# Kernel tuning notes

Hardware: AMD Instinct MI355X
Metric: run time of the kernel (lower is better)

The kernel has to match this reference:

```python
import jax, jax.numpy as jnp
import numpy as np

B, N, C, H, NRES = 32, 1024, 384, 1024, 20
NTAB = 21  # 20 aa + unknown, per AlphaFold residue_constants


def setup_inputs() -> dict:
    key = jax.random.key(0)
    ks = jax.random.split(key, 16)
    s = 0.02
    inp = {}
    inp['act'] = jax.random.normal(ks[0], (B, N, C), jnp.float32)
    inp['angles'] = jax.random.normal(ks[1], (B, N, 7, 2), jnp.float32)
    inp['rigids'] = jax.random.normal(ks[2], (B, N, 7), jnp.float32)
    inp['fixed_mask'] = jax.random.randint(ks[3], (B, N), 0, 2, jnp.int32)
    inp['seq_t'] = jax.random.randint(ks[4], (B, N), 0, NRES, jnp.int32)
    inp['residx_atom37_to_atom14'] = jax.random.randint(ks[5], (B, N, 37), 0, 14, jnp.int32)
    inp['ln_g'] = jnp.ones((C,), jnp.float32)
    inp['ln_b'] = jnp.zeros((C,), jnp.float32)
    inp['w1'] = jax.random.normal(ks[6], (C, H), jnp.float32) * s
    inp['b1'] = jnp.zeros((H,), jnp.float32)
    inp['w2'] = jax.random.normal(ks[7], (H, H), jnp.float32) * s
    inp['b2'] = jnp.zeros((H,), jnp.float32)
    inp['w3'] = jax.random.normal(ks[8], (H, NRES), jnp.float32) * s
    inp['b3'] = jnp.zeros((NRES,), jnp.float32)
    # stand-in residue_constants tables (same shapes/dtypes as AlphaFold's)
    inp['default_frames'] = jax.random.normal(ks[9], (NTAB, 8, 4, 4), jnp.float32)
    inp['group_idx'] = jax.random.randint(ks[10], (NTAB, 14), 0, 8, jnp.int32)
    inp['atom14_mask'] = (jax.random.uniform(ks[11], (NTAB, 14)) > 0.3).astype(jnp.float32)
    inp['atom37_mask'] = (jax.random.uniform(ks[12], (NTAB, 37)) > 0.3).astype(jnp.float32)
    inp['lit_positions'] = jax.random.normal(ks[13], (NTAB, 14, 3), jnp.float32)
    return inp


def quat_to_rot(q):
    q = q / jnp.sqrt(jnp.sum(q * q, axis=-1, keepdims=True) + 1e-8)
    w, x, y, z = q[..., 0], q[..., 1], q[..., 2], q[..., 3]
    r = jnp.stack([
        1 - 2 * (y * y + z * z), 2 * (x * y - w * z), 2 * (x * z + w * y),
        2 * (x * y + w * z), 1 - 2 * (x * x + z * z), 2 * (y * z - w * x),
        2 * (x * z - w * y), 2 * (y * z + w * x), 1 - 2 * (x * x + y * y)
    ], axis=-1)
    return r.reshape(q.shape[:-1] + (3, 3))


def compose(r1, t1, r2, t2):
    # rigid composition: (r1, t1) o (r2, t2)
    return (jnp.einsum('...ij,...jk->...ik', r1, r2),
            jnp.einsum('...ij,...j->...i', r1, t2) + t1)


def reference(act, angles, rigids, fixed_mask, seq_t, residx_atom37_to_atom14,
              ln_g, ln_b, w1, b1, w2, b2, w3, b3,
              default_frames, group_idx, atom14_mask, atom37_mask, lit_positions):
    # --- small MLP head ---
    mu = jnp.mean(act, axis=-1, keepdims=True)
    var = jnp.var(act, axis=-1, keepdims=True)
    h = (act - mu) / jnp.sqrt(var + 1e-5) * ln_g + ln_b
    h = jax.nn.relu(h @ w1 + b1)
    h = jax.nn.relu(h @ w2 + b2)
    logits = h @ w3 + b3                                # [B,N,20]
    p_0t = jax.nn.softmax(logits, axis=-1)
    seq0 = jnp.argmax(p_0t, axis=-1).astype(jnp.int32)
    seq0 = seq0 * (1 - fixed_mask) + seq_t * fixed_mask  # [B,N]

    # --- backbone frame from quaternion rigids ---
    rb = quat_to_rot(rigids[..., :4])                    # [B,N,3,3]
    tb = rigids[..., 4:]                                 # [B,N,3]

    # --- torsion_angles_to_frames ---
    df = default_frames[seq0]                            # [B,N,8,4,4]
    dr, dt = df[..., :3, :3], df[..., :3, 3]
    sin, cos = angles[..., 0], angles[..., 1]            # [B,N,7]
    z1 = jnp.zeros_like(sin[..., :1])
    sin8 = jnp.concatenate([z1, sin], axis=-1)           # backbone group has angle 0
    cos8 = jnp.concatenate([jnp.ones_like(z1), cos], axis=-1)
    zz, oo = jnp.zeros_like(sin8), jnp.ones_like(sin8)
    rx = jnp.stack([oo, zz, zz, zz, cos8, -sin8, zz, sin8, cos8], axis=-1)
    rx = rx.reshape(sin8.shape + (3, 3))                 # rotation about x-axis
    fr = jnp.einsum('bngij,bngjk->bngik', dr, rx)        # frames to backbone (pre-chain)
    ft = dt
    # chain chi2->chi1, chi3->chi2, chi4->chi3
    r5, t5 = compose(fr[..., 4, :, :], ft[..., 4, :], fr[..., 5, :, :], ft[..., 5, :])
    r6, t6 = compose(r5, t5, fr[..., 6, :, :], ft[..., 6, :])
    r7, t7 = compose(r6, t6, fr[..., 7, :, :], ft[..., 7, :])
    frot = jnp.concatenate([fr[..., :5, :, :], r5[..., None, :, :], r6[..., None, :, :], r7[..., None, :, :]], axis=-3)
    ftr = jnp.concatenate([ft[..., :5, :], t5[..., None, :], t6[..., None, :], t7[..., None, :]], axis=-2)
    grot, gtr = compose(rb[..., None, :, :], tb[..., None, :], frot, ftr)  # [B,N,8,3,3],[B,N,8,3]

    # --- frames_and_literature_positions_to_atom14_pos ---
    gi = group_idx[seq0]                                 # [B,N,14]
    ar = jnp.take_along_axis(grot, jnp.broadcast_to(gi[..., None, None], gi.shape + (3, 3)), axis=2)
    at = jnp.take_along_axis(gtr, jnp.broadcast_to(gi[..., None], gi.shape + (3,)), axis=2)
    lit = lit_positions[seq0]                            # [B,N,14,3]
    m14 = atom14_mask[seq0]                              # [B,N,14]
    pred = (jnp.einsum('bnaij,bnaj->bnai', ar, lit) + at) * m14[..., None]

    # --- atom14 -> atom37 gather ---
    idx = residx_atom37_to_atom14
    final = jnp.take_along_axis(pred, jnp.broadcast_to(idx[..., None], idx.shape + (3,)), axis=2)
    m37 = atom37_mask[seq0]                              # [B,N,37]
    return logits, seq0, pred, final, m14, m37
```

## Files before the change

### kernel.cpp

```cpp
#include <hip/hip_runtime.h>
#include <math.h>

#define B_ 32
#define N_ 1024
#define C_ 384
#define H_ 1024
#define NRES 20
#define NTAB 21
#define M_TOTAL (B_*N_)
#define BK 32

typedef __attribute__((ext_vector_type(8))) short bf16x8;
typedef __attribute__((ext_vector_type(4))) float f32x4;

#define GLOAD_LDS(gptr, lptr) \
    __builtin_amdgcn_global_load_lds( \
        (const __attribute__((address_space(1))) void*)(gptr), \
        (__attribute__((address_space(3))) void*)(lptr), 16, 0, 0)

__device__ inline short bf16_rne(float v) {
    unsigned u = __float_as_uint(v);
    unsigned r = u + 0x7fffu + ((u >> 16) & 1u);
    return (short)(r >> 16);
}
__device__ inline void split2(float v, short& h, short& l) {
    unsigned u = __float_as_uint(v);
    unsigned r = (u + 0x7fffu + ((u >> 16) & 1u)) & 0xffff0000u;
    h = (short)(r >> 16);
    l = bf16_rne(v - __uint_as_float(r));
}

__global__ __launch_bounds__(256) void ln_split_kernel(const float* __restrict__ act,
                                                       const float* __restrict__ lng,
                                                       const float* __restrict__ lnb,
                                                       short* __restrict__ Xh,
                                                       short* __restrict__ Xl) {
    int wave = threadIdx.x >> 6;
    int lane = threadIdx.x & 63;
    int row  = blockIdx.x * 4 + wave;
    const float* x = act + (size_t)row * C_;
    float v[6];
    float s = 0.f;
#pragma unroll
    for (int i = 0; i < 6; i++) { v[i] = x[lane + i*64]; s += v[i]; }
#pragma unroll
    for (int off = 32; off > 0; off >>= 1) s += __shfl_xor(s, off, 64);
    float mu = s * (1.0f/384.0f);
    float vs = 0.f;
#pragma unroll
    for (int i = 0; i < 6; i++) { float d = v[i]-mu; vs += d*d; }
#pragma unroll
    for (int off = 32; off > 0; off >>= 1) vs += __shfl_xor(vs, off, 64);
    float rstd = 1.0f / sqrtf(vs * (1.0f/384.0f) + 1e-5f);
#pragma unroll
    for (int i = 0; i < 6; i++) {
        int col = lane + i*64;
        float y = (v[i] - mu) * rstd * lng[col] + lnb[col];
        short h, l; split2(y, h, l);
        Xh[(size_t)row * C_ + col] = h;
        Xl[(size_t)row * C_ + col] = l;
    }
}

__global__ __launch_bounds__(256) void conv_w_kernel(const float* __restrict__ w,
                                                     short* __restrict__ th,
                                                     short* __restrict__ tl,
                                                     int K, int N, int Npad) {
    __shared__ float t[32][33];
    int n0 = blockIdx.x * 32, k0 = blockIdx.y * 32;
    int tx = threadIdx.x & 31, ty = threadIdx.x >> 5;
#pragma unroll
    for (int i = ty; i < 32; i += 8) {
        int k = k0 + i, n = n0 + tx;
        t[i][tx] = (n < N) ? w[(size_t)k * N + n] : 0.f;
    }
    __syncthreads();
#pragma unroll
    for (int i = ty; i < 32; i += 8) {
        int n = n0 + i, k = k0 + tx;
        short h, l; split2(t[tx][i], h, l);
        th[(size_t)n * K + k] = h;
        tl[(size_t)n * K + k] = l;
    }
}

__global__ __launch_bounds__(256) void presplit_gemm128(
    const short* __restrict__ Ahg, const short* __restrict__ Alg,
    const short* __restrict__ BTh, const short* __restrict__ BTl,
    const float* __restrict__ bias,
    short* __restrict__ Ch, short* __restrict__ Cl,
    int K, int ldc)
{
    __shared__ short Ah[2][128][32], Al[2][128][32], Bh[2][128][32], Bl[2][128][32];
    int tid = threadIdx.x;
    int m0 = blockIdx.x * 128;
    int n0 = blockIdx.y * 128;
    int lane = tid & 63, wv = tid >> 6;
    int wm = (wv & 1) * 64, wn = (wv >> 1) * 64;
    int fm = lane & 15, kg = lane >> 4;

    const short* gsrc = (wv == 0) ? Ahg : (wv == 1) ? Alg : (wv == 2) ? BTh : BTl;
    short* lb0 = (wv == 0) ? &Ah[0][0][0] : (wv == 1) ? &Al[0][0][0]
               : (wv == 2) ? &Bh[0][0][0] : &Bl[0][0][0];
    int base = (wv < 2) ? m0 : n0;
    int swcb = (lane & 3) ^ ((lane >> 3) & 3);
    const short* gp = gsrc + (size_t)(base + (lane >> 2)) * K + swcb * 8;

    int sa[4], sb[4];
#pragma unroll
    for (int i = 0; i < 4; i++) {
        int ra = wm + i*16 + fm;
        int rb = wn + i*16 + fm;
        sa[i] = (kg ^ ((ra >> 1) & 3)) * 8;
        sb[i] = (kg ^ ((rb >> 1) & 3)) * 8;
    }

    f32x4 acc[4][4] = {};
    const int NT = K / BK;

#pragma unroll
    for (int c = 0; c < 8; c++)
        GLOAD_LDS(gp + (size_t)(c * 16) * K, lb0 + c * 512);

    for (int t = 0; t < NT; ++t) {
        __syncthreads();

        if (t + 1 < NT) {
            short* lb = lb0 + ((t + 1) & 1) * (128 * 32);
            size_t k0n = (size_t)(t + 1) * BK;
#pragma unroll
            for (int c = 0; c < 8; c++)
                GLOAD_LDS(gp + (size_t)(c * 16) * K + k0n, lb + c * 512);
        }

        int cur = t & 1;
        bf16x8 a_h[4], a_l[4], b_h[4], b_l[4];
#pragma unroll
        for (int i = 0; i < 4; i++) {
            a_h[i] = *(bf16x8*)&Ah[cur][wm + i*16 + fm][sa[i]];
            a_l[i] = *(bf16x8*)&Al[cur][wm + i*16 + fm][sa[i]];
            b_h[i] = *(bf16x8*)&Bh[cur][wn + i*16 + fm][sb[i]];
            b_l[i] = *(bf16x8*)&Bl[cur][wn + i*16 + fm][sb[i]];
        }
#pragma unroll
        for (int i = 0; i < 4; i++)
#pragma unroll
            for (int j = 0; j < 4; j++) {
                f32x4 c = acc[i][j];
                c = __builtin_amdgcn_mfma_f32_16x16x32_bf16(a_l[i], b_h[j], c, 0, 0, 0);
                c = __builtin_amdgcn_mfma_f32_16x16x32_bf16(a_h[i], b_l[j], c, 0, 0, 0);
                c = __builtin_amdgcn_mfma_f32_16x16x32_bf16(a_h[i], b_h[j], c, 0, 0, 0);
                acc[i][j] = c;
            }
    }

#pragma unroll
    for (int i = 0; i < 4; i++)
#pragma unroll
        for (int j = 0; j < 4; j++) {
            int col = n0 + wn + j*16 + fm;
            float bs = bias[col];
#pragma unroll
            for (int r = 0; r < 4; r++) {
                int row = m0 + wm + i*16 + kg*4 + r;
                float v = fmaxf(acc[i][j][r] + bs, 0.f);
                short h, l; split2(v, h, l);
                Ch[(size_t)row * ldc + col] = h;
                Cl[(size_t)row * ldc + col] = l;
            }
        }
}

__global__ __launch_bounds__(256) void gemm3_fused(
    const short* __restrict__ Ahg, const short* __restrict__ Alg,
    const short* __restrict__ BTh, const short* __restrict__ BTl,
    const float* __restrict__ b3,
    const int* __restrict__ fixed_mask, const int* __restrict__ seq_t,
    float* __restrict__ out_logits, float* __restrict__ seq_out,
    int* __restrict__ seq_int, int m0c)
{
    __shared__ short Ah[2][64][32], Al[2][64][32];
    __shared__ short Bh[2][32][32], Bl[2][32][32];
    __shared__ float slog[64][33];
    int tid = threadIdx.x;
    int m0 = blockIdx.x * 64;
    int lane = tid & 63, wv = tid >> 6;
    int wm = wv * 16;
    int fm = lane & 15, kg = lane >> 4;

    const short* gsrc = (wv == 0) ? Ahg : (wv == 1) ? Alg : (wv == 2) ? BTh : BTl;
    short* lb0 = (wv == 0) ? &Ah[0][0][0] : (wv == 1) ? &Al[0][0][0]
               : (wv == 2) ? &Bh[0][0][0] : &Bl[0][0][0];
    int pstride = (wv < 2) ? (64*32) : (32*32);
    int ncalls  = (wv < 2) ? 4 : 2;
    int base = (wv < 2) ? m0 : 0;
    int swcb = (lane & 3) ^ ((lane >> 3) & 3);
    const short* gp = gsrc + (size_t)(base + (lane >> 2)) * H_ + swcb * 8;

    int saz = (kg ^ (((wm + fm) >> 1) & 3)) * 8;
    int sbz[2];
#pragma unroll
    for (int j = 0; j < 2; j++) sbz[j] = (kg ^ (((j*16 + fm) >> 1) & 3)) * 8;

    f32x4 acc[2] = {};
    const int NT = H_ / BK;

    for (int c = 0; c < ncalls; c++)
        GLOAD_LDS(gp + (size_t)(c * 16) * H_, lb0 + c * 512);

    for (int t = 0; t < NT; ++t) {
        __syncthreads();

        if (t + 1 < NT) {
            short* lb = lb0 + ((t + 1) & 1) * pstride;
            size_t k0n = (size_t)(t + 1) * BK;
            for (int c = 0; c < ncalls; c++)
                GLOAD_LDS(gp + (size_t)(c * 16) * H_ + k0n, lb + c * 512);
        }

        int cur = t & 1;
        bf16x8 a_h = *(bf16x8*)&Ah[cur][wm + fm][saz];
        bf16x8 a_l = *(bf16x8*)&Al[cur][wm + fm][saz];
        bf16x8 b_h[2], b_l[2];
#pragma unroll
        for (int j = 0; j < 2; j++) {
            b_h[j] = *(bf16x8*)&Bh[cur][j*16 + fm][sbz[j]];
            b_l[j] = *(bf16x8*)&Bl[cur][j*16 + fm][sbz[j]];
        }
#pragma unroll
        for (int j = 0; j < 2; j++) {
            f32x4 c = acc[j];
            c = __builtin_amdgcn_mfma_f32_16x16x32_bf16(a_l, b_h[j], c, 0, 0, 0);
            c = __builtin_amdgcn_mfma_f32_16x16x32_bf16(a_h, b_l[j], c, 0, 0, 0);
            c = __builtin_amdgcn_mfma_f32_16x16x32_bf16(a_h, b_h[j], c, 0, 0, 0);
            acc[j] = c;
        }
    }

#pragma unroll
    for (int j = 0; j < 2; j++)
#pragma unroll
        for (int r = 0; r < 4; r++)
            slog[wm + kg*4 + r][j*16 + fm] = acc[j][r];
    __syncthreads();

    if (tid < 64) {
        int grow = m0c + m0 + tid;
        float best = -1e30f; int bi = 0;
        float* lg = out_logits + (size_t)grow * NRES;
#pragma unroll
        for (int n = 0; n < NRES; n++) {
            float s = slog[tid][n] + b3[n];
            lg[n] = s;
            if (s > best) { best = s; bi = n; }
        }
        int fmk = fixed_mask[grow];
        int s = fmk ? seq_t[grow] : bi;
        seq_int[grow] = s;
        seq_out[grow] = (float)s;
    }
}

__global__ __launch_bounds__(128) void geom_kernel(
    const float* __restrict__ angles, const float* __restrict__ rigids,
    const int* __restrict__ seq0i, const int* __restrict__ residx,
    const float* __restrict__ dframes, const int* __restrict__ gidx,
    const float* __restrict__ a14m, const float* __restrict__ a37m,
    const float* __restrict__ litp,
    float* __restrict__ out_pred, float* __restrict__ out_final,
    float* __restrict__ out_m14, float* __restrict__ out_m37)
{
    __shared__ float sdf[NTAB*8*16];
    __shared__ int   sgi[NTAB*14];
    __shared__ float sm14[NTAB*14];
    __shared__ float sm37[NTAB*37];
    __shared__ float slit[NTAB*14*3];
    __shared__ float predL[128][43];

    for (int i = threadIdx.x; i < NTAB*128; i += 128) sdf[i] = dframes[i];
    for (int i = threadIdx.x; i < NTAB*14; i += 128) { sgi[i] = gidx[i]; sm14[i] = a14m[i]; }
    for (int i = threadIdx.x; i < NTAB*37; i += 128) sm37[i] = a37m[i];
    for (int i = threadIdx.x; i < NTAB*42; i += 128) slit[i] = litp[i];
    __syncthreads();

    int p = blockIdx.x * 128 + threadIdx.x;
    int s = seq0i[p];

    const float* rg = rigids + (size_t)p * 7;
    float qw = rg[0], qx = rg[1], qy = rg[2], qz = rg[3];
    float tbx = rg[4], tby = rg[5], tbz = rg[6];
    float qn = 1.0f / sqrtf(qw*qw + qx*qx + qy*qy + qz*qz + 1e-8f);
    qw *= qn; qx *= qn; qy *= qn; qz *= qn;
    float rb[9];
    rb[0] = 1.f - 2.f*(qy*qy + qz*qz); rb[1] = 2.f*(qx*qy - qw*qz); rb[2] = 2.f*(qx*qz + qw*qy);
    rb[3] = 2.f*(qx*qy + qw*qz); rb[4] = 1.f - 2.f*(qx*qx + qz*qz); rb[5] = 2.f*(qy*qz - qw*qx);
    rb[6] = 2.f*(qx*qz - qw*qy); rb[7] = 2.f*(qy*qz + qw*qx); rb[8] = 1.f - 2.f*(qx*qx + qy*qy);

    float fr[8][9], ft[8][3];
    const float* ang = angles + (size_t)p * 14;
#pragma unroll
    for (int g = 0; g < 8; g++) {
        const float* df = &sdf[(s*8 + g)*16];
        float c, sn;
        if (g == 0) { c = 1.f; sn = 0.f; }
        else { sn = ang[(g-1)*2 + 0]; c = ang[(g-1)*2 + 1]; }
#pragma unroll
        for (int i = 0; i < 3; i++) {
            float d0 = df[i*4+0], d1 = df[i*4+1], d2 = df[i*4+2];
            fr[g][i*3+0] = d0;
            fr[g][i*3+1] = d1*c + d2*sn;
            fr[g][i*3+2] = d2*c - d1*sn;
            ft[g][i] = df[i*4+3];
        }
    }
#pragma unroll
    for (int g = 5; g <= 7; g++) {
        float r[9], t[3];
        const float* r1 = fr[g-1];
        const float* t1 = ft[g-1];
#pragma unroll
        for (int i = 0; i < 3; i++) {
#pragma unroll
            for (int j = 0; j < 3; j++)
                r[i*3+j] = r1[i*3+0]*fr[g][0*3+j] + r1[i*3+1]*fr[g][1*3+j] + r1[i*3+2]*fr[g][2*3+j];
            t[i] = r1[i*3+0]*ft[g][0] + r1[i*3+1]*ft[g][1] + r1[i*3+2]*ft[g][2] + t1[i];
        }
#pragma unroll
        for (int i = 0; i < 9; i++) fr[g][i] = r[i];
#pragma unroll
        for (int i = 0; i < 3; i++) ft[g][i] = t[i];
    }
#pragma unroll
    for (int g = 0; g < 8; g++) {
        float r[9], t[3];
#pragma unroll
        for (int i = 0; i < 3; i++) {
#pragma unroll
            for (int j = 0; j < 3; j++)
                r[i*3+j] = rb[i*3+0]*fr[g][0*3+j] + rb[i*3+1]*fr[g][1*3+j] + rb[i*3+2]*fr[g][2*3+j];
            t[i] = rb[i*3+0]*ft[g][0] + rb[i*3+1]*ft[g][1] + rb[i*3+2]*ft[g][2];
        }
#pragma unroll
        for (int i = 0; i < 9; i++) fr[g][i] = r[i];
        ft[g][0]=t[0]+tbx; ft[g][1]=t[1]+tby; ft[g][2]=t[2]+tbz;
    }
#pragma unroll
    for (int g = 0; g < 8; g++) {
#pragma unroll
        for (int a = 0; a < 14; a++) {
            if (sgi[s*14 + a] == g) {
                float m  = sm14[s*14 + a];
                float lx = slit[(s*14 + a)*3 + 0];
                float ly = slit[(s*14 + a)*3 + 1];
                float lz = slit[(s*14 + a)*3 + 2];
                float px = (fr[g][0]*lx + fr[g][1]*ly + fr[g][2]*lz + ft[g][0]) * m;
                float py = (fr[g][3]*lx + fr[g][4]*ly + fr[g][5]*lz + ft[g][1]) * m;
                float pz = (fr[g][6]*lx + fr[g][7]*ly + fr[g][8]*lz + ft[g][2]) * m;
                predL[threadIdx.x][a*3+0] = px;
                predL[threadIdx.x][a*3+1] = py;
                predL[threadIdx.x][a*3+2] = pz;
                out_pred[((size_t)p*14 + a)*3 + 0] = px;
                out_pred[((size_t)p*14 + a)*3 + 1] = py;
                out_pred[((size_t)p*14 + a)*3 + 2] = pz;
            }
        }
    }
#pragma unroll
    for (int a = 0; a < 14; a++) out_m14[(size_t)p*14 + a] = sm14[s*14 + a];

    const int* idx = residx + (size_t)p * 37;
#pragma unroll
    for (int a = 0; a < 37; a++) {
        int id = idx[a];
        out_final[((size_t)p*37 + a)*3 + 0] = predL[threadIdx.x][id*3+0];
        out_final[((size_t)p*37 + a)*3 + 1] = predL[threadIdx.x][id*3+1];
        out_final[((size_t)p*37 + a)*3 + 2] = predL[threadIdx.x][id*3+2];
        out_m37[(size_t)p*37 + a] = sm37[s*37 + a];
    }
}

extern "C" void kernel_launch(void* const* d_in, const int* in_sizes, int n_in,
                              void* d_out, int out_size, void* d_ws, size_t ws_size,
                              hipStream_t stream) {
    const float* act        = (const float*)d_in[0];
    const float* angles     = (const float*)d_in[1];
    const float* rigids     = (const float*)d_in[2];
    const int*   fixed_mask = (const int*)d_in[3];
    const int*   seq_t      = (const int*)d_in[4];
    const int*   residx     = (const int*)d_in[5];
    const float* lng        = (const float*)d_in[6];
    const float* lnb        = (const float*)d_in[7];
    const float* w1         = (const float*)d_in[8];
    const float* b1         = (const float*)d_in[9];
    const float* w2         = (const float*)d_in[10];
    const float* b2         = (const float*)d_in[11];
    const float* w3         = (const float*)d_in[12];
    const float* b3         = (const float*)d_in[13];
    const float* dfr        = (const float*)d_in[14];
    const int*   gidx       = (const int*)d_in[15];
    const float* a14m       = (const float*)d_in[16];
    const float* a37m       = (const float*)d_in[17];
    const float* litp       = (const float*)d_in[18];

    float* out        = (float*)d_out;
    float* out_logits = out;
    float* out_seq    = out_logits + (size_t)M_TOTAL * NRES;
    float* out_pred   = out_seq    + (size_t)M_TOTAL;
    float* out_final  = out_pred   + (size_t)M_TOTAL * 42;
    float* out_m14    = out_final  + (size_t)M_TOTAL * 111;
    float* out_m37    = out_m14    + (size_t)M_TOTAL * 14;

    char* wsp = (char*)d_ws;
    int*   seq0i = (int*)wsp;   wsp += (size_t)M_TOTAL * sizeof(int);
    short* w1h   = (short*)wsp; wsp += (size_t)H_ * C_ * sizeof(short);
    short* w1l   = (short*)wsp; wsp += (size_t)H_ * C_ * sizeof(short);
    short* w2h   = (short*)wsp; wsp += (size_t)H_ * H_ * sizeof(short);
    short* w2l   = (short*)wsp; wsp += (size_t)H_ * H_ * sizeof(short);
    short* w3h   = (short*)wsp; wsp += (size_t)128 * H_ * sizeof(short);
    short* w3l   = (short*)wsp; wsp += (size_t)128 * H_ * sizeof(short);
    short* Xh    = (short*)wsp; wsp += (size_t)M_TOTAL * C_ * sizeof(short);
    short* Xl    = (short*)wsp; wsp += (size_t)M_TOTAL * C_ * sizeof(short);

    size_t fixed_bytes = (size_t)(wsp - (char*)d_ws);
    size_t per_row = 4ull * H_ * sizeof(short);
    size_t avail = ws_size - fixed_bytes;
    int chunkM = 4096;
    if (avail >= (size_t)M_TOTAL * per_row)      chunkM = M_TOTAL;
    else if (avail >= 16384ull * per_row)        chunkM = 16384;
    else if (avail >= 8192ull * per_row)         chunkM = 8192;

    short* H1h = (short*)wsp; wsp += (size_t)chunkM * H_ * sizeof(short);
    short* H1l = (short*)wsp; wsp += (size_t)chunkM * H_ * sizeof(short);
    short* H2h = (short*)wsp; wsp += (size_t)chunkM * H_ * sizeof(short);
    short* H2l = (short*)wsp;

    conv_w_kernel<<<dim3(H_/32, C_/32), 256, 0, stream>>>(w1, w1h, w1l, C_, H_, H_);
    conv_w_kernel<<<dim3(H_/32, H_/32), 256, 0, stream>>>(w2, w2h, w2l, H_, H_, H_);
    conv_w_kernel<<<dim3(128/32, H_/32), 256, 0, stream>>>(w3, w3h, w3l, H_, NRES, 128);

    ln_split_kernel<<<M_TOTAL/4, 256, 0, stream>>>(act, lng, lnb, Xh, Xl);

    for (int c = 0; c < M_TOTAL / chunkM; c++) {
        int m0 = c * chunkM;
        presplit_gemm128<<<dim3(chunkM/128, H_/128), 256, 0, stream>>>(
            Xh + (size_t)m0 * C_, Xl + (size_t)m0 * C_, w1h, w1l, b1, H1h, H1l, C_, H_);
        presplit_gemm128<<<dim3(chunkM/128, H_/128), 256, 0, stream>>>(
            H1h, H1l, w2h, w2l, b2, H2h, H2l, H_, H_);
        gemm3_fused<<<chunkM/64, 256, 0, stream>>>(H2h, H2l, w3h, w3l, b3,
                                                   fixed_mask, seq_t,
                                                   out_logits, out_seq, seq0i, m0);
    }

    geom_kernel<<<M_TOTAL/128, 128, 0, stream>>>(angles, rigids, seq0i, residx,
                                                 dfr, gidx, a14m, a37m, litp,
                                                 out_pred, out_final, out_m14, out_m37);
}
```

Baseline: 499.7 us.

## Enlarge split-bf16 GEMM tile to 256x256 with phased prefetch and setprio

Replaces the 128x128 four-wave GEMM with a 256x256 eight-wave kernel where each wave computes a 128x64 sub-tile. Global-to-LDS loads for the next K-slice are split into four phases interleaved with MFMA clusters, separated by explicit barriers, vmcnt waits and s_setprio raises. The goal is more operand reuse per LDS byte and better overlap of loads with the triple-MFMA compute. In exchange the kernel uses more LDS and registers per block, has more barriers, and launches fewer blocks.

```diff
diff --git a/kernel.cpp b/kernel.cpp
--- a/kernel.cpp
+++ b/kernel.cpp
@@ -84,91 +84,142 @@
     }
 }
 
-__global__ __launch_bounds__(256) void presplit_gemm128(
+__global__ __launch_bounds__(512, 2) void presplit_gemm256(
     const short* __restrict__ Ahg, const short* __restrict__ Alg,
     const short* __restrict__ BTh, const short* __restrict__ BTl,
     const float* __restrict__ bias,
     short* __restrict__ Ch, short* __restrict__ Cl,
     int K, int ldc)
 {
-    __shared__ short Ah[2][128][32], Al[2][128][32], Bh[2][128][32], Bl[2][128][32];
+    __shared__ short P[4][2][256][32];
+    const int BUFS = 256*32;
     int tid = threadIdx.x;
-    int m0 = blockIdx.x * 128;
-    int n0 = blockIdx.y * 128;
+    int m0 = blockIdx.x * 256;
+    int n0 = blockIdx.y * 256;
     int lane = tid & 63, wv = tid >> 6;
-    int wm = (wv & 1) * 64, wn = (wv >> 1) * 64;
+    int wr = wv >> 2, wc = wv & 3;
     int fm = lane & 15, kg = lane >> 4;
 
-    const short* gsrc = (wv == 0) ? Ahg : (wv == 1) ? Alg : (wv == 2) ? BTh : BTl;
-    short* lb0 = (wv == 0) ? &Ah[0][0][0] : (wv == 1) ? &Al[0][0][0]
-               : (wv == 2) ? &Bh[0][0][0] : &Bl[0][0][0];
-    int base = (wv < 2) ? m0 : n0;
+    int pl = wv >> 1, hf = wv & 1;
+    const short* gsrc = (pl == 0) ? Ahg : (pl == 1) ? Alg : (pl == 2) ? BTh : BTl;
+    int base = (pl < 2) ? m0 : n0;
     int swcb = (lane & 3) ^ ((lane >> 3) & 3);
-    const short* gp = gsrc + (size_t)(base + (lane >> 2)) * K + swcb * 8;
-
-    int sa[4], sb[4];
-#pragma unroll
-    for (int i = 0; i < 4; i++) {
-        int ra = wm + i*16 + fm;
-        int rb = wn + i*16 + fm;
-        sa[i] = (kg ^ ((ra >> 1) & 3)) * 8;
-        sb[i] = (kg ^ ((rb >> 1) & 3)) * 8;
-    }
-
-    f32x4 acc[4][4] = {};
+    const short* gp = gsrc + (size_t)(base + hf*128 + (lane >> 2)) * K + swcb * 8;
+    short* lpl = &P[pl][0][0][0] + hf * (128*32);
+
+    int sz = (kg ^ ((fm >> 1) & 3)) * 8;
+    const short* raH = &P[0][0][wr*128 + fm][0] + sz;
+    const short* raL = &P[1][0][wr*128 + fm][0] + sz;
+    const short* rbH = &P[2][0][wc*64  + fm][0] + sz;
+    const short* rbL = &P[3][0][wc*64  + fm][0] + sz;
+
+#define STAGE(c, bsel, koff) \
+    GLOAD_LDS(gp + (size_t)((c)*16) * K + (koff), lpl + (bsel)*BUFS + (c)*512)
+
+#define TRIPLE(ai, aj, AH, AL, BH, BL) { \
+    f32x4 cc = acc[ai][aj]; \
+    cc = __builtin_amdgcn_mfma_f32_16x16x32_bf16(AL, BH, cc, 0, 0, 0); \
+    cc = __builtin_amdgcn_mfma_f32_16x16x32_bf16(AH, BL, cc, 0, 0, 0); \
+    cc = __builtin_amdgcn_mfma_f32_16x16x32_bf16(AH, BH, cc, 0, 0, 0); \
+    acc[ai][aj] = cc; }
+
+    f32x4 acc[8][4] = {};
     const int NT = K / BK;
 
 #pragma unroll
-    for (int c = 0; c < 8; c++)
-        GLOAD_LDS(gp + (size_t)(c * 16) * K, lb0 + c * 512);
+    for (int c = 0; c < 8; c++) STAGE(c, 0, 0);
 
     for (int t = 0; t < NT; ++t) {
-        __syncthreads();
-
-        if (t + 1 < NT) {
-            short* lb = lb0 + ((t + 1) & 1) * (128 * 32);
-            size_t k0n = (size_t)(t + 1) * BK;
-#pragma unroll
-            for (int c = 0; c < 8; c++)
-                GLOAD_LDS(gp + (size_t)(c * 16) * K + k0n, lb + c * 512);
-        }
-
-        int cur = t & 1;
+        int cur = t & 1, nxt = cur ^ 1;
+        size_t koff = (size_t)(t + 1) * BK;
+        bool pf = (t + 1 < NT);
+
         bf16x8 a_h[4], a_l[4], b_h[4], b_l[4];
+
+        if (pf) {
+            STAGE(0, nxt, koff); STAGE(1, nxt, koff);
+            asm volatile("s_waitcnt vmcnt(2)" ::: "memory");
+        } else {
+            asm volatile("s_waitcnt vmcnt(0)" ::: "memory");
+        }
+        __builtin_amdgcn_s_barrier();
+        __builtin_amdgcn_sched_barrier(0);
 #pragma unroll
         for (int i = 0; i < 4; i++) {
-            a_h[i] = *(bf16x8*)&Ah[cur][wm + i*16 + fm][sa[i]];
-            a_l[i] = *(bf16x8*)&Al[cur][wm + i*16 + fm][sa[i]];
-            b_h[i] = *(bf16x8*)&Bh[cur][wn + i*16 + fm][sb[i]];
-            b_l[i] = *(bf16x8*)&Bl[cur][wn + i*16 + fm][sb[i]];
-        }
+            a_h[i] = *(const bf16x8*)(raH + cur*BUFS + i*512);
+            a_l[i] = *(const bf16x8*)(raL + cur*BUFS + i*512);
+        }
+#pragma unroll
+        for (int j = 0; j < 2; j++) {
+            b_h[j] = *(const bf16x8*)(rbH + cur*BUFS + j*512);
+            b_l[j] = *(const bf16x8*)(rbL + cur*BUFS + j*512);
+        }
+        __builtin_amdgcn_s_setprio(1);
 #pragma unroll
         for (int i = 0; i < 4; i++)
 #pragma unroll
-            for (int j = 0; j < 4; j++) {
-                f32x4 c = acc[i][j];
-                c = __builtin_amdgcn_mfma_f32_16x16x32_bf16(a_l[i], b_h[j], c, 0, 0, 0);
-                c = __builtin_amdgcn_mfma_f32_16x16x32_bf16(a_h[i], b_l[j], c, 0, 0, 0);
-                c = __builtin_amdgcn_mfma_f32_16x16x32_bf16(a_h[i], b_h[j], c, 0, 0, 0);
-                acc[i][j] = c;
-            }
-    }
-
-#pragma unroll
-    for (int i = 0; i < 4; i++)
+            for (int j = 0; j < 2; j++) TRIPLE(i, j, a_h[i], a_l[i], b_h[j], b_l[j]);
+        __builtin_amdgcn_s_setprio(0);
+        __builtin_amdgcn_s_barrier();
+
+        if (pf) { STAGE(2, nxt, koff); STAGE(3, nxt, koff); }
+#pragma unroll
+        for (int j = 0; j < 2; j++) {
+            b_h[2+j] = *(const bf16x8*)(rbH + cur*BUFS + (2+j)*512);
+            b_l[2+j] = *(const bf16x8*)(rbL + cur*BUFS + (2+j)*512);
+        }
+        __builtin_amdgcn_s_barrier();
+        __builtin_amdgcn_s_setprio(1);
+#pragma unroll
+        for (int i = 0; i < 4; i++)
+#pragma unroll
+            for (int j = 0; j < 2; j++) TRIPLE(i, 2+j, a_h[i], a_l[i], b_h[2+j], b_l[2+j]);
+        __builtin_amdgcn_s_setprio(0);
+        __builtin_amdgcn_s_barrier();
+
+        if (pf) { STAGE(4, nxt, koff); STAGE(5, nxt, koff); }
+#pragma unroll
+        for (int i = 0; i < 4; i++) {
+            a_h[i] = *(const bf16x8*)(raH + cur*BUFS + (4+i)*512);
+            a_l[i] = *(const bf16x8*)(raL + cur*BUFS + (4+i)*512);
+        }
+        __builtin_amdgcn_s_barrier();
+        __builtin_amdgcn_s_setprio(1);
+#pragma unroll
+        for (int i = 0; i < 4; i++)
+#pragma unroll
+            for (int j = 0; j < 2; j++) TRIPLE(4+i, j, a_h[i], a_l[i], b_h[j], b_l[j]);
+        __builtin_amdgcn_s_setprio(0);
+        __builtin_amdgcn_s_barrier();
+
+        if (pf) { STAGE(6, nxt, koff); STAGE(7, nxt, koff); }
+        __builtin_amdgcn_s_barrier();
+        __builtin_amdgcn_s_setprio(1);
+#pragma unroll
+        for (int i = 0; i < 4; i++)
+#pragma unroll
+            for (int j = 0; j < 2; j++) TRIPLE(4+i, 2+j, a_h[i], a_l[i], b_h[2+j], b_l[2+j]);
+        __builtin_amdgcn_s_setprio(0);
+        __builtin_amdgcn_s_barrier();
+    }
+
+#pragma unroll
+    for (int i = 0; i < 8; i++)
 #pragma unroll
         for (int j = 0; j < 4; j++) {
-            int col = n0 + wn + j*16 + fm;
+            int col = n0 + wc*64 + j*16 + fm;
             float bs = bias[col];
 #pragma unroll
             for (int r = 0; r < 4; r++) {
-                int row = m0 + wm + i*16 + kg*4 + r;
+                int row = m0 + wr*128 + i*16 + kg*4 + r;
                 float v = fmaxf(acc[i][j][r] + bs, 0.f);
                 short h, l; split2(v, h, l);
                 Ch[(size_t)row * ldc + col] = h;
                 Cl[(size_t)row * ldc + col] = l;
             }
         }
+#undef STAGE
+#undef TRIPLE
 }
 
 __global__ __launch_bounds__(256) void gemm3_fused(
@@ -442,9 +493,9 @@
 
     for (int c = 0; c < M_TOTAL / chunkM; c++) {
         int m0 = c * chunkM;
-        presplit_gemm128<<<dim3(chunkM/128, H_/128), 256, 0, stream>>>(
+        presplit_gemm256<<<dim3(chunkM/256, H_/256), 512, 0, stream>>>(
             Xh + (size_t)m0 * C_, Xl + (size_t)m0 * C_, w1h, w1l, b1, H1h, H1l, C_, H_);
-        presplit_gemm128<<<dim3(chunkM/128, H_/128), 256, 0, stream>>>(
+        presplit_gemm256<<<dim3(chunkM/256, H_/256), 512, 0, stream>>>(
             H1h, H1l, w2h, w2l, b2, H2h, H2l, H_, H_);
         gemm3_fused<<<chunkM/64, 256, 0, stream>>>(H2h, H2l, w3h, w3l, b3,
                                                    fixed_mask, seq_t,
```

Measured after the change: 462.9 us. 1.08x faster.
